# Performance work log

Measured on AMD Instinct MI355X. Metric: run time of the kernel, lower is better.

The kernel has to match this reference:

```python
import jax, jax.numpy as jnp
import numpy as np

INIT_L = 512.0
EPS = 1e-6
N_HEAD = 16


def fire_bias(T, w1, b1, w2, b2, c, L_multiplier):
    # positions and relative distances
    pos = jnp.arange(T, dtype=jnp.float32)
    rel = pos[:, None] - pos[None, :]                      # (T, T)
    threshold = jnp.abs(L_multiplier * INIT_L)
    pos_norm = jnp.maximum(pos, threshold)[:, None]        # (T, 1)
    rel = jnp.log(jnp.abs(c * rel) + 1.0)                  # (T, T)
    pos_norm = jnp.log(jnp.abs(c * pos_norm) + 1.0) + EPS  # (T, 1)
    nd = rel / pos_norm                                    # (T, T)
    # tiny MLP: 1 -> mlp_width -> n_head
    h = jax.nn.relu(nd[..., None] * w1[0] + b1)            # (T, T, 32)
    bias = jnp.einsum('tsw,wh->hts', h, w2) + b2[:, None, None]  # (H, T, T)
    causal = jnp.tril(jnp.ones((T, T), dtype=bool))
    bias = jnp.where(causal[None], bias, -jnp.inf)
    return bias[None]                                      # (1, H, T, T)


def reference(x, Wqkv, bqkv, Wproj, bproj, w1, b1, w2, b2, c_param, L_multiplier):
    B, T, C = x.shape
    H = N_HEAD
    hd = C // H
    qkv = x @ Wqkv + bqkv                                  # (B, T, 3C)
    q, k, v = jnp.split(qkv, 3, axis=-1)
    q = q.reshape(B, T, H, hd).transpose(0, 2, 1, 3)       # (B, H, T, hd)
    k = k.reshape(B, T, H, hd).transpose(0, 2, 1, 3)
    v = v.reshape(B, T, H, hd).transpose(0, 2, 1, 3)
    bias = fire_bias(T, w1, b1, w2, b2, c_param, L_multiplier)  # (1, H, T, T)
    scale = 1.0 / jnp.sqrt(jnp.float32(hd))
    att = jnp.einsum('bhqd,bhkd->bhqk', q, k) * scale + bias
    att = jax.nn.softmax(att, axis=-1)
    y = jnp.einsum('bhqk,bhkd->bhqd', att, v)              # (B, H, T, hd)
    y = y.transpose(0, 2, 1, 3).reshape(B, T, C)
    return y @ Wproj + bproj


def setup_inputs() -> dict:
    key = jax.random.key(0)
    ks = jax.random.split(key, 8)
    B, T, C, H, W = 2, 2048, 1024, 16, 32
    s = 0.02
    return {
        'x': jax.random.normal(ks[0], (B, T, C), jnp.float32),
        'Wqkv': jax.random.normal(ks[1], (C, 3 * C), jnp.float32) * s,
        'bqkv': jnp.zeros((3 * C,), jnp.float32),
        'Wproj': jax.random.normal(ks[2], (C, C), jnp.float32) * s,
        'bproj': jnp.zeros((C,), jnp.float32),
        'w1': jax.random.normal(ks[3], (1, W), jnp.float32),
        'b1': jnp.zeros((W,), jnp.float32),
        'w2': jax.random.normal(ks[4], (W, H), jnp.float32) * 0.1,
        'b2': jnp.zeros((H,), jnp.float32),
        'c_param': jnp.float32(0.1),
        'L_multiplier': jnp.float32(1.0),
    }
```

## Files before the change

kernel.cpp:

```cpp
#include <hip/hip_runtime.h>
#include <cstdint>

typedef unsigned short u16;
typedef unsigned int u32;

typedef short bf16x8 __attribute__((ext_vector_type(8)));
typedef float f32x4 __attribute__((ext_vector_type(4)));

#define LN2 0.69314718055994530942f
#define LOG2E 1.44269504088896340736f
#define INFF __builtin_inff()

__device__ __forceinline__ u16 f2bf(float f) {
  u32 u = __float_as_uint(f);
  u = (u + 0x7fffu + ((u >> 16) & 1u)) >> 16;
  return (u16)u;
}
__device__ __forceinline__ u32 pack2bf(float a, float b) {
  u32 ta = __float_as_uint(a) + 0x8000u;
  u32 tb = __float_as_uint(b) + 0x8000u;
  return __builtin_amdgcn_perm(tb, ta, 0x07060302u);
}

#if __has_builtin(__builtin_amdgcn_global_load_lds)
#define HAVE_GLDS 1
__device__ __forceinline__ void glds16(const u16* g, u16* l) {
  __builtin_amdgcn_global_load_lds((const __attribute__((address_space(1))) void*)g,
                                   (__attribute__((address_space(3))) void*)l, 16, 0, 0);
}
#else
#define HAVE_GLDS 0
#endif

__device__ __forceinline__ u16* swzp(u16* base, int row, int bc) {
  return (u16*)((char*)base + row * 128 + (bc ^ ((row & 7) << 4)));
}


__global__ void k_convert_x(const float* __restrict__ in, u16* __restrict__ out, int n4) {
  int i = blockIdx.x * blockDim.x + threadIdx.x;
  if (i < n4) {
    float4 v = ((const float4*)in)[i];
    ushort4 o;
    o.x = f2bf(v.x); o.y = f2bf(v.y); o.z = f2bf(v.z); o.w = f2bf(v.w);
    ((ushort4*)out)[i] = o;
  }
}

__global__ void k_transpose_bf(const float* __restrict__ in, u16* __restrict__ out, int R, int C) {
  __shared__ float t[32][33];
  int c0 = blockIdx.x * 32, r0 = blockIdx.y * 32;
  int tx = threadIdx.x, ty = threadIdx.y;
#pragma unroll
  for (int k = 0; k < 4; k++) t[ty + 8 * k][tx] = in[(size_t)(r0 + ty + 8 * k) * C + c0 + tx];
  __syncthreads();
#pragma unroll
  for (int k = 0; k < 4; k++) out[(size_t)(c0 + ty + 8 * k) * R + r0 + tx] = f2bf(t[tx][ty + 8 * k]);
}

__global__ void k_tables(const float* __restrict__ cP, const float* __restrict__ lP,
                         float* __restrict__ ig2, float* __restrict__ rl) {
  int t = blockIdx.x * blockDim.x + threadIdx.x;
  float c = fabsf(cP[0]);
  if (t < 2048) {
    float lm = lP[0];
    float thr = fabsf(lm * 512.0f);
    float pn = fmaxf((float)t, thr);
    float den = logf(c * pn + 1.0f) + 1e-6f;
    ig2[t] = LN2 / den;
  }
  if (t < 2112) {
    int d = t - 63;
    if (d < 0) d = 0;
    rl[t] = log2f(c * (float)d + 1.0f);
  }
}

__global__ void k_segments(const float* __restrict__ w1, const float* __restrict__ b1,
                           const float* __restrict__ w2, const float* __restrict__ b2,
                           float* __restrict__ segX, float* __restrict__ segA,
                           float* __restrict__ segB, int* __restrict__ segU) {
  __shared__ float xs[32];
  __shared__ float srt[32];
  __shared__ float uniq[32];
  __shared__ int uCnt;
  int t = threadIdx.x;
  if (t < 32) {
    float w = w1[t], b = b1[t];
    xs[t] = (w != 0.0f) ? (-b / w) : INFF;
  }
  __syncthreads();
  if (t < 32) {
    float x = xs[t];
    int r = 0;
    for (int v = 0; v < 32; v++) {
      float xv = xs[v];
      if (xv < x || (xv == x && v < t)) r++;
    }
    srt[r] = x;
  }
  __syncthreads();
  if (t == 0) {
    int u = 0;
    for (int i = 0; i < 32; i++) {
      float v = srt[i];
      if (v < 3.0e38f && (u == 0 || v != uniq[u - 1])) uniq[u++] = v;
    }
    uCnt = u;
    segU[0] = u;
  }
  __syncthreads();
  int u = uCnt;
  if (t < u) segX[t] = uniq[t];
  for (int idx = t; idx < (u + 1) * 16; idx += blockDim.x) {
    int j = idx >> 4, h = idx & 15;
    float p;
    if (u == 0) p = 0.0f;
    else if (j == 0) p = uniq[0] - 1.0f;
    else if (j == u) p = uniq[u - 1] + 1.0f;
    else p = 0.5f * (uniq[j - 1] + uniq[j]);
    float A = b2[h], B = 0.0f;
    for (int w = 0; w < 32; w++) {
      float w1w = w1[w], b1w = b1[w], w2wh = w2[w * 16 + h];
      if (w1w != 0.0f) {
        if (fmaf(w1w, p, b1w) > 0.0f) { B += w1w * w2wh; A += b1w * w2wh; }
      } else if (b1w > 0.0f) {
        A += b1w * w2wh;
      }
    }
    segA[j * 16 + h] = A;
    segB[j * 16 + h] = B;
  }
}

template <int MODE, int BN>
__launch_bounds__(256, 3)
__global__ void k_gemm(const u16* __restrict__ A, const u16* __restrict__ BT,
                       const float* __restrict__ bias, float* __restrict__ outF,
                       u16* __restrict__ outQ, u16* __restrict__ outK, u16* __restrict__ outV,
                       int M, int N, int K) {
  constexpr int NT = BN / 32;
  constexpr int NCH = BN / 32;
  __shared__ u16 As[128 * 64];
  __shared__ u16 Bs[BN * 64];
  const int tid = threadIdx.x;
  const int lane = tid & 63, wave = tid >> 6;
  const int li = lane & 15, quad = lane >> 4;
  const int wrow = (wave >> 1) * 64, wcol = (wave & 1) * (BN / 2);
  const int rb = blockIdx.y * 128, cb = blockIdx.x * BN;

  f32x4 acc[4][NT];
#pragma unroll
  for (int i = 0; i < 4; i++)
#pragma unroll
    for (int j = 0; j < NT; j++) acc[i][j] = (f32x4){0.f, 0.f, 0.f, 0.f};

#if HAVE_GLDS
  const u16* gA = A + (size_t)(rb + (tid >> 3)) * K + (tid & 7) * 8;
  const u16* gB = BT + (size_t)(cb + (tid >> 3)) * K + (tid & 7) * 8;
  u16* lA = As + wave * 512;
  u16* lB = Bs + wave * 512;

  for (int k0 = 0; k0 < K; k0 += 64) {
    __syncthreads();
#pragma unroll
    for (int ch = 0; ch < 4; ch++) glds16(gA + (size_t)ch * 32 * K + k0, lA + ch * 2048);
#pragma unroll
    for (int ch = 0; ch < NCH; ch++) glds16(gB + (size_t)ch * 32 * K + k0, lB + ch * 2048);
    __syncthreads();
#pragma unroll
    for (int c = 0; c < 2; c++) {
      bf16x8 af[4], bfr[NT];
#pragma unroll
      for (int mt = 0; mt < 4; mt++)
        af[mt] = *(const bf16x8*)(&As[(wrow + mt * 16 + li) * 64 + c * 32 + quad * 8]);
#pragma unroll
      for (int nt = 0; nt < NT; nt++)
        bfr[nt] = *(const bf16x8*)(&Bs[(wcol + nt * 16 + li) * 64 + c * 32 + quad * 8]);
#pragma unroll
      for (int mt = 0; mt < 4; mt++)
#pragma unroll
        for (int nt = 0; nt < NT; nt++)
          acc[mt][nt] = __builtin_amdgcn_mfma_f32_16x16x32_bf16(af[mt], bfr[nt], acc[mt][nt], 0, 0, 0);
    }
  }
#else
  for (int k0 = 0; k0 < K; k0 += 64) {
    __syncthreads();
    for (int idx = tid * 8; idx < 128 * 64; idx += 256 * 8) {
      int rr = idx >> 6, cc = idx & 63;
      *(uint4*)(&As[idx]) = *(const uint4*)(A + (size_t)(rb + rr) * K + k0 + cc);
    }
    for (int idx = tid * 8; idx < BN * 64; idx += 256 * 8) {
      int rr = idx >> 6, cc = idx & 63;
      *(uint4*)(&Bs[idx]) = *(const uint4*)(BT + (size_t)(cb + rr) * K + k0 + cc);
    }
    __syncthreads();
#pragma unroll
    for (int c = 0; c < 2; c++) {
      bf16x8 af[4], bfr[NT];
#pragma unroll
      for (int mt = 0; mt < 4; mt++)
        af[mt] = *(const bf16x8*)(&As[(wrow + mt * 16 + li) * 64 + c * 32 + quad * 8]);
#pragma unroll
      for (int nt = 0; nt < NT; nt++)
        bfr[nt] = *(const bf16x8*)(&Bs[(wcol + nt * 16 + li) * 64 + c * 32 + quad * 8]);
#pragma unroll
      for (int mt = 0; mt < 4; mt++)
#pragma unroll
        for (int nt = 0; nt < NT; nt++)
          acc[mt][nt] = __builtin_amdgcn_mfma_f32_16x16x32_bf16(af[mt], bfr[nt], acc[mt][nt], 0, 0, 0);
    }
  }
#endif

#pragma unroll
  for (int mt = 0; mt < 4; mt++)
#pragma unroll
    for (int nt = 0; nt < NT; nt++)
#pragma unroll
      for (int r = 0; r < 4; r++) {
        int row = rb + wrow + mt * 16 + quad * 4 + r;
        int col = cb + wcol + nt * 16 + li;
        float v = acc[mt][nt][r] + bias[col];
        if (MODE == 0) {
          int b = row >> 11, tt = row & 2047;
          int sel = col >> 10, w = col & 1023, h = w >> 6, dd = w & 63;
          u16* dst = (sel == 0) ? outQ : ((sel == 1) ? outK : outV);
          dst[(size_t)((b * 16 + h) * 2048 + tt) * 64 + dd] = f2bf(v);
        } else {
          outF[(size_t)row * N + col] = v;
        }
      }
}

__launch_bounds__(256, 3)
__global__ void k_attn(const u16* __restrict__ Q, const u16* __restrict__ K,
                       const u16* __restrict__ V, u16* __restrict__ Y,
                       const float* __restrict__ ig2, const float* __restrict__ RL,
                       const float* __restrict__ segX, const float* __restrict__ segA,
                       const float* __restrict__ segB, const int* __restrict__ segU) {
  __shared__ u16 Ks[64 * 64];
  __shared__ u16 Vts[64 * 64];
  __shared__ u16 Ps[64 * 64];
  __shared__ float rls[2112];
  __shared__ float sXl[32];
  __shared__ float sAl[33];
  __shared__ float sBl[33];

  const int xi = blockIdx.x, h = blockIdx.y, b = blockIdx.z;
  const int q0b = xi >> 1;
  const int flip = (xi & 1) ^ ((h >> 3) & 1);
  const int qt = flip ? (31 - q0b) : q0b;

  const int tid = threadIdx.x, lane = tid & 63, wave = tid >> 6;
  const int li = lane & 15, quad = lane >> 4;
  const int bh = b * 16 + h;
  const u16* Qg = Q + (size_t)bh * 2048 * 64;
  const u16* Kg = K + (size_t)bh * 2048 * 64;
  const u16* Vg = V + (size_t)bh * 2048 * 64;

  for (int i = tid; i < 2112; i += 256) rls[i] = RL[i];

  const int u = segU[0];
  float x0 = INFF, A0, B0, A1, B1;
  A0 = segA[h]; B0 = segB[h]; A1 = A0; B1 = B0;
  if (u == 1) { x0 = segX[0]; A1 = segA[16 + h]; B1 = segB[16 + h]; }
  if (u > 1) {
    if (tid < u) sXl[tid] = segX[tid];
    if (tid < u + 1) { sAl[tid] = segA[tid * 16 + h]; sBl[tid] = segB[tid * 16 + h]; }
  }
  const float A0e = A0 * LOG2E, A1e = A1 * LOG2E;
  const float SCL = 0.125f * LOG2E;

  const int qw = qt * 64 + wave * 16;
  const int t = qw + li;
  bf16x8 qf[2];
#pragma unroll
  for (int c = 0; c < 2; c++)
    qf[c] = *(const bf16x8*)(Qg + (size_t)t * 64 + c * 32 + quad * 8);

  const float gI = ig2[t];
  const float x0r = x0 / gI;
  const float B0g = B0 * gI * LOG2E, B1g = B1 * gI * LOG2E;
  float mrow = -INFF, lrow = 0.0f;
  f32x4 oacc[4];
#pragma unroll
  for (int nt = 0; nt < 4; nt++) oacc[nt] = (f32x4){0.f, 0.f, 0.f, 0.f};

  uint4 kv0, kv1, w0, w1;
  {
    const u16* ksrc = Kg + (size_t)(tid >> 2) * 64 + (tid & 3) * 16;
    kv0 = *(const uint4*)(ksrc);
    kv1 = *(const uint4*)(ksrc + 8);
    const u16* vsrc = Vg + (size_t)(2 * (tid & 31)) * 64 + (tid >> 5) * 8;
    w0 = *(const uint4*)(vsrc);
    w1 = *(const uint4*)(vsrc + 64);
  }

  const int krow = tid >> 2, kcol = (tid & 3) * 32;
  const int kkp = tid & 31, d0v = (tid >> 5) * 8;

  for (int kt = 0; kt <= qt; kt++) {
    const int kb = kt * 64;
    __syncthreads();
    *(uint4*)swzp(Ks, krow, kcol) = kv0;
    *(uint4*)swzp(Ks, krow, kcol + 16) = kv1;
    {
      const u16* pw0 = (const u16*)&w0;
      const u16* pw1 = (const u16*)&w1;
#pragma unroll
      for (int j = 0; j < 8; j++)
        *(u32*)swzp(Vts, d0v + j, 4 * kkp) = (u32)pw0[j] | ((u32)pw1[j] << 16);
    }
    __syncthreads();
    if (kt < qt) {
      const u16* ksrc = Kg + (size_t)(kb + 64 + (tid >> 2)) * 64 + (tid & 3) * 16;
      kv0 = *(const uint4*)(ksrc);
      kv1 = *(const uint4*)(ksrc + 8);
      const u16* vsrc = Vg + (size_t)(kb + 64 + 2 * (tid & 31)) * 64 + (tid >> 5) * 8;
      w0 = *(const uint4*)(vsrc);
      w1 = *(const uint4*)(vsrc + 64);
    }

    f32x4 sacc[4];
#pragma unroll
    for (int nt = 0; nt < 4; nt++) sacc[nt] = (f32x4){0.f, 0.f, 0.f, 0.f};
#pragma unroll
    for (int c = 0; c < 2; c++)
#pragma unroll
      for (int nt = 0; nt < 4; nt++) {
        bf16x8 kf = *(const bf16x8*)swzp(Ks, nt * 16 + li, c * 64 + quad * 16);
        sacc[nt] = __builtin_amdgcn_mfma_f32_16x16x32_bf16(kf, qf[c], sacc[nt], 0, 0, 0);
      }

    const int Cbase = t - kb - quad * 4 + 63;
    const float* rp = &rls[Cbase - 51];
    if (u <= 1) {
      const int lim = Cbase - 63;
#pragma unroll
      for (int nt = 0; nt < 4; nt++)
#pragma unroll
        for (int r = 0; r < 4; r++) {
          float rlv = rp[51 - nt * 16 - r];
          bool hi = rlv > x0r;
          float z = fmaf(rlv, hi ? B1g : B0g, hi ? A1e : A0e);
          z = fmaf(sacc[nt][r], SCL, z);
          if (kt == qt) z = (nt * 16 + r > lim) ? -INFF : z;
          sacc[nt][r] = z;
        }
    } else {
      const int lim = Cbase - 63;
#pragma unroll
      for (int nt = 0; nt < 4; nt++)
#pragma unroll
        for (int r = 0; r < 4; r++) {
          float nd = rp[51 - nt * 16 - r] * gI;
          int j = 0;
          for (int i = 0; i < u; i++) j += (nd > sXl[i]) ? 1 : 0;
          float z = (fmaf(nd, sBl[j], sAl[j]) + sacc[nt][r] * 0.125f) * LOG2E;
          if (kt == qt) z = (nt * 16 + r > lim) ? -INFF : z;
          sacc[nt][r] = z;
        }
    }

    f32x4 mm = sacc[0];
#pragma unroll
    for (int nt = 1; nt < 4; nt++)
#pragma unroll
      for (int r = 0; r < 4; r++) mm[r] = fmaxf(mm[r], sacc[nt][r]);
    float vm = fmaxf(fmaxf(mm[0], mm[1]), fmaxf(mm[2], mm[3]));
    vm = fmaxf(vm, __shfl_xor(vm, 16, 64));
    vm = fmaxf(vm, __shfl_xor(vm, 32, 64));
    float mnew = fmaxf(mrow, vm);
    bool grew = mnew > mrow;
    float alpha = __builtin_amdgcn_exp2f(mrow - mnew);
    mrow = mnew;
#pragma unroll
    for (int nt = 0; nt < 4; nt++)
#pragma unroll
      for (int r = 0; r < 4; r++)
        sacc[nt][r] = __builtin_amdgcn_exp2f(sacc[nt][r] - mnew);
    f32x4 sv = (sacc[0] + sacc[1]) + (sacc[2] + sacc[3]);
    float s = (sv[0] + sv[1]) + (sv[2] + sv[3]);
    s += __shfl_xor(s, 16, 64);
    s += __shfl_xor(s, 32, 64);
    lrow = lrow * alpha + s;
    if (__any(grew)) {
#pragma unroll
      for (int nt = 0; nt < 4; nt++)
#pragma unroll
        for (int r = 0; r < 4; r++) oacc[nt][r] *= alpha;
    }

    const int prow = wave * 16 + li;
#pragma unroll
    for (int nt = 0; nt < 4; nt++) {
      uint2 pk;
      pk.x = pack2bf(sacc[nt][0], sacc[nt][1]);
      pk.y = pack2bf(sacc[nt][2], sacc[nt][3]);
      *(uint2*)swzp(Ps, prow, 32 * nt + 8 * quad) = pk;
    }

#pragma unroll
    for (int c = 0; c < 2; c++) {
      bf16x8 pf = *(const bf16x8*)swzp(Ps, prow, c * 64 + quad * 16);
#pragma unroll
      for (int nt = 0; nt < 4; nt++) {
        bf16x8 vf = *(const bf16x8*)swzp(Vts, nt * 16 + li, c * 64 + quad * 16);
        oacc[nt] = __builtin_amdgcn_mfma_f32_16x16x32_bf16(vf, pf, oacc[nt], 0, 0, 0);
      }
    }
  }

  float inv = 1.0f / lrow;
  u16* dst = Y + (size_t)(b * 2048 + t) * 1024 + h * 64 + quad * 4;
#pragma unroll
  for (int nt = 0; nt < 4; nt++) {
    uint2 pk;
    pk.x = pack2bf(oacc[nt][0] * inv, oacc[nt][1] * inv);
    pk.y = pack2bf(oacc[nt][2] * inv, oacc[nt][3] * inv);
    *(uint2*)(dst + nt * 16) = pk;
  }
}

extern "C" void kernel_launch(void* const* d_in, const int* in_sizes, int n_in,
                              void* d_out, int out_size, void* d_ws, size_t ws_size,
                              hipStream_t stream) {
  (void)in_sizes; (void)n_in; (void)out_size; (void)ws_size;
  const float* x = (const float*)d_in[0];
  const float* Wqkv = (const float*)d_in[1];
  const float* bqkv = (const float*)d_in[2];
  const float* Wproj = (const float*)d_in[3];
  const float* bproj = (const float*)d_in[4];
  const float* w1 = (const float*)d_in[5];
  const float* b1 = (const float*)d_in[6];
  const float* w2 = (const float*)d_in[7];
  const float* b2 = (const float*)d_in[8];
  const float* cP = (const float*)d_in[9];
  const float* lP = (const float*)d_in[10];

  char* ws = (char*)d_ws;
  u16* Xbf = (u16*)(ws);
  u16* WqkvT = (u16*)(ws + (size_t)(8 << 20));
  u16* WprojT = (u16*)(ws + (size_t)(14 << 20));
  u16* Qb = (u16*)(ws + (size_t)(16 << 20));
  u16* Kb = (u16*)(ws + (size_t)(24 << 20));
  u16* Vb = (u16*)(ws + (size_t)(32 << 20));
  u16* Yb = (u16*)(ws + (size_t)(40 << 20));
  float* IG = (float*)(ws + (size_t)(48 << 20));
  float* RL = IG + 2048;
  float* SEGX = RL + 2112;
  float* SEGA = SEGX + 32;
  float* SEGB = SEGA + 33 * 16;
  int* SEGU = (int*)(SEGB + 33 * 16);

  k_convert_x<<<4096, 256, 0, stream>>>(x, Xbf, 1048576);
  k_transpose_bf<<<dim3(96, 32), dim3(32, 8), 0, stream>>>(Wqkv, WqkvT, 1024, 3072);
  k_transpose_bf<<<dim3(32, 32), dim3(32, 8), 0, stream>>>(Wproj, WprojT, 1024, 1024);
  k_tables<<<9, 256, 0, stream>>>(cP, lP, IG, RL);
  k_segments<<<1, 64, 0, stream>>>(w1, b1, w2, b2, SEGX, SEGA, SEGB, SEGU);

  k_gemm<0, 128><<<dim3(24, 32), 256, 0, stream>>>(Xbf, WqkvT, bqkv, nullptr, Qb, Kb, Vb,
                                                   4096, 3072, 1024);
  k_attn<<<dim3(32, 16, 2), 256, 0, stream>>>(Qb, Kb, Vb, Yb, IG, RL, SEGX, SEGA, SEGB, SEGU);
  k_gemm<1, 64><<<dim3(16, 32), 256, 0, stream>>>(Yb, WprojT, bproj, (float*)d_out, nullptr,
                                                  nullptr, nullptr, 4096, 1024, 1024);
}
```

Baseline: 243.8 us.

## Split long causal attention query tiles across two blocks with a combine pass

Query tiles 16-31 are now split along the key dimension into two blocks. Each block writes unnormalized fp32 partial outputs plus max and sum statistics, and a new combine kernel merges them into the bf16 output. Short tiles still run as single blocks, so the grid grows from 1024 to 1536 blocks and the work per block is more even, which shortens the tail from the longest causal rows. The cost is an extra kernel launch, fp32 partial traffic through workspace memory, and WprojT moving in the workspace because PO reuses the Xbf region.

```diff
diff --git a/kernel.cpp b/kernel.cpp
--- a/kernel.cpp
+++ b/kernel.cpp
@@ -237,6 +237,7 @@
 __launch_bounds__(256, 3)
 __global__ void k_attn(const u16* __restrict__ Q, const u16* __restrict__ K,
                        const u16* __restrict__ V, u16* __restrict__ Y,
+                       float* __restrict__ PO, float* __restrict__ ML,
                        const float* __restrict__ ig2, const float* __restrict__ RL,
                        const float* __restrict__ segX, const float* __restrict__ segA,
                        const float* __restrict__ segB, const int* __restrict__ segU) {
@@ -249,9 +250,21 @@
   __shared__ float sBl[33];
 
   const int xi = blockIdx.x, h = blockIdx.y, b = blockIdx.z;
-  const int q0b = xi >> 1;
-  const int flip = (xi & 1) ^ ((h >> 3) & 1);
-  const int qt = flip ? (31 - q0b) : q0b;
+  int qt, k0, k1, half, split;
+  if (xi < 32) {
+    qt = 31 - (xi >> 1);
+    half = xi & 1;
+    split = 1;
+    const int h0 = (qt + 2) >> 1;
+    k0 = half ? h0 : 0;
+    k1 = half ? (qt + 1) : h0;
+  } else {
+    qt = 47 - xi;
+    half = 0;
+    split = 0;
+    k0 = 0;
+    k1 = qt + 1;
+  }
 
   const int tid = threadIdx.x, lane = tid & 63, wave = tid >> 6;
   const int li = lane & 15, quad = lane >> 4;
@@ -290,10 +303,10 @@
 
   uint4 kv0, kv1, w0, w1;
   {
-    const u16* ksrc = Kg + (size_t)(tid >> 2) * 64 + (tid & 3) * 16;
+    const u16* ksrc = Kg + (size_t)(k0 * 64 + (tid >> 2)) * 64 + (tid & 3) * 16;
     kv0 = *(const uint4*)(ksrc);
     kv1 = *(const uint4*)(ksrc + 8);
-    const u16* vsrc = Vg + (size_t)(2 * (tid & 31)) * 64 + (tid >> 5) * 8;
+    const u16* vsrc = Vg + (size_t)(k0 * 64 + 2 * (tid & 31)) * 64 + (tid >> 5) * 8;
     w0 = *(const uint4*)(vsrc);
     w1 = *(const uint4*)(vsrc + 64);
   }
@@ -301,7 +314,7 @@
   const int krow = tid >> 2, kcol = (tid & 3) * 32;
   const int kkp = tid & 31, d0v = (tid >> 5) * 8;
 
-  for (int kt = 0; kt <= qt; kt++) {
+  for (int kt = k0; kt < k1; kt++) {
     const int kb = kt * 64;
     __syncthreads();
     *(uint4*)swzp(Ks, krow, kcol) = kv0;
@@ -314,7 +327,7 @@
         *(u32*)swzp(Vts, d0v + j, 4 * kkp) = (u32)pw0[j] | ((u32)pw1[j] << 16);
     }
     __syncthreads();
-    if (kt < qt) {
+    if (kt + 1 < k1) {
       const u16* ksrc = Kg + (size_t)(kb + 64 + (tid >> 2)) * 64 + (tid & 3) * 16;
       kv0 = *(const uint4*)(ksrc);
       kv1 = *(const uint4*)(ksrc + 8);
@@ -413,15 +426,56 @@
     }
   }
 
-  float inv = 1.0f / lrow;
-  u16* dst = Y + (size_t)(b * 2048 + t) * 1024 + h * 64 + quad * 4;
-#pragma unroll
-  for (int nt = 0; nt < 4; nt++) {
-    uint2 pk;
-    pk.x = pack2bf(oacc[nt][0] * inv, oacc[nt][1] * inv);
-    pk.y = pack2bf(oacc[nt][2] * inv, oacc[nt][3] * inv);
-    *(uint2*)(dst + nt * 16) = pk;
-  }
+  if (split) {
+    const int p = bh * 32 + (qt - 16) * 2 + half;
+    const int qr = wave * 16 + li;
+    float* po = PO + (size_t)p * 4096 + (size_t)qr * 64 + quad * 4;
+#pragma unroll
+    for (int nt = 0; nt < 4; nt++) {
+      float4 v4 = make_float4(oacc[nt][0], oacc[nt][1], oacc[nt][2], oacc[nt][3]);
+      *(float4*)(po + nt * 16) = v4;
+    }
+    if (quad == 0) {
+      ML[p * 128 + qr * 2] = mrow;
+      ML[p * 128 + qr * 2 + 1] = lrow;
+    }
+  } else {
+    float inv = 1.0f / lrow;
+    u16* dst = Y + (size_t)(b * 2048 + t) * 1024 + h * 64 + quad * 4;
+#pragma unroll
+    for (int nt = 0; nt < 4; nt++) {
+      uint2 pk;
+      pk.x = pack2bf(oacc[nt][0] * inv, oacc[nt][1] * inv);
+      pk.y = pack2bf(oacc[nt][2] * inv, oacc[nt][3] * inv);
+      *(uint2*)(dst + nt * 16) = pk;
+    }
+  }
+}
+
+__global__ void k_combine(const float* __restrict__ PO, const float* __restrict__ ML,
+                          u16* __restrict__ Y) {
+  const int gid = blockIdx.x * 256 + threadIdx.x;
+  const int d4 = gid & 15;
+  const int row = (gid >> 4) & 1023;
+  const int bh = gid >> 14;
+  const int qt16 = row >> 6, r = row & 63;
+  const int p0 = bh * 32 + qt16 * 2;
+  const float* o0 = PO + (size_t)p0 * 4096 + (size_t)r * 64 + d4 * 4;
+  const float* o1 = o0 + 4096;
+  const float m0 = ML[p0 * 128 + r * 2], l0 = ML[p0 * 128 + r * 2 + 1];
+  const float m1 = ML[(p0 + 1) * 128 + r * 2], l1 = ML[(p0 + 1) * 128 + r * 2 + 1];
+  const float m = fmaxf(m0, m1);
+  const float e0 = __builtin_amdgcn_exp2f(m0 - m);
+  const float e1 = __builtin_amdgcn_exp2f(m1 - m);
+  const float inv = 1.0f / (l0 * e0 + l1 * e1);
+  const float4 a = *(const float4*)o0;
+  const float4 c = *(const float4*)o1;
+  const int t = 1024 + row, b = bh >> 4, h = bh & 15;
+  u16* dst = Y + (size_t)(b * 2048 + t) * 1024 + h * 64 + d4 * 4;
+  uint2 pk;
+  pk.x = pack2bf(fmaf(a.x, e0, c.x * e1) * inv, fmaf(a.y, e0, c.y * e1) * inv);
+  pk.y = pack2bf(fmaf(a.z, e0, c.z * e1) * inv, fmaf(a.w, e0, c.w * e1) * inv);
+  *(uint2*)dst = pk;
 }
 
 extern "C" void kernel_launch(void* const* d_in, const int* in_sizes, int n_in,
@@ -443,7 +497,6 @@
   char* ws = (char*)d_ws;
   u16* Xbf = (u16*)(ws);
   u16* WqkvT = (u16*)(ws + (size_t)(8 << 20));
-  u16* WprojT = (u16*)(ws + (size_t)(14 << 20));
   u16* Qb = (u16*)(ws + (size_t)(16 << 20));
   u16* Kb = (u16*)(ws + (size_t)(24 << 20));
   u16* Vb = (u16*)(ws + (size_t)(32 << 20));
@@ -454,6 +507,9 @@
   float* SEGA = SEGX + 32;
   float* SEGB = SEGA + 33 * 16;
   int* SEGU = (int*)(SEGB + 33 * 16);
+  u16* WprojT = (u16*)(ws + (size_t)(49 << 20));
+  float* PO = (float*)(ws);
+  float* ML = (float*)(ws + (size_t)(51 << 20));
 
   k_convert_x<<<4096, 256, 0, stream>>>(x, Xbf, 1048576);
   k_transpose_bf<<<dim3(96, 32), dim3(32, 8), 0, stream>>>(Wqkv, WqkvT, 1024, 3072);
@@ -463,7 +519,9 @@
 
   k_gemm<0, 128><<<dim3(24, 32), 256, 0, stream>>>(Xbf, WqkvT, bqkv, nullptr, Qb, Kb, Vb,
                                                    4096, 3072, 1024);
-  k_attn<<<dim3(32, 16, 2), 256, 0, stream>>>(Qb, Kb, Vb, Yb, IG, RL, SEGX, SEGA, SEGB, SEGU);
+  k_attn<<<dim3(48, 16, 2), 256, 0, stream>>>(Qb, Kb, Vb, Yb, PO, ML, IG, RL, SEGX, SEGA,
+                                              SEGB, SEGU);
+  k_combine<<<2048, 256, 0, stream>>>(PO, ML, Yb);
   k_gemm<1, 64><<<dim3(16, 32), 256, 0, stream>>>(Yb, WprojT, bproj, (float*)d_out, nullptr,
                                                   nullptr, nullptr, 4096, 1024, 1024);
 }
```

Result: no change. 246.0 us (+0.9%).

## Pre-swizzle K and transpose V in GEMM epilogue; double-buffer attention tiles via direct LDS loads

Applied to the files above, without the earlier changes.

The QKV GEMM epilogue now writes K with an XOR swizzle and V already transposed and swizzled, so the attention kernel can copy tiles straight from global memory into LDS with global_load_lds instead of staging them through registers and scattering. K and V LDS buffers are doubled so the next tile loads while the current one is computed, and one of the two __syncthreads per iteration goes away. A specialized bias path skips the piecewise select when both segments are effectively the same. The change raises LDS use per block, which may reduce occupancy, and relies on the epilogue layout matching the swizzle the attention kernel reads with.

```diff
diff --git a/kernel.cpp b/kernel.cpp
--- a/kernel.cpp
+++ b/kernel.cpp
@@ -20,6 +20,9 @@
   u32 ta = __float_as_uint(a) + 0x8000u;
   u32 tb = __float_as_uint(b) + 0x8000u;
   return __builtin_amdgcn_perm(tb, ta, 0x07060302u);
+}
+__device__ __forceinline__ u32 pack2bf_rne(float a, float b) {
+  return (u32)f2bf(a) | ((u32)f2bf(b) << 16);
 }
 
 #if __has_builtin(__builtin_amdgcn_global_load_lds)
@@ -31,6 +34,15 @@
 #else
 #define HAVE_GLDS 0
 #endif
+
+__device__ __forceinline__ void stage1k(const u16* gperlane, u16* lwave, int lane) {
+#if HAVE_GLDS
+  (void)lane;
+  glds16(gperlane, lwave);
+#else
+  *(uint4*)(lwave + lane * 8) = *(const uint4*)gperlane;
+#endif
+}
 
 __device__ __forceinline__ u16* swzp(u16* base, int row, int bc) {
   return (u16*)((char*)base + row * 128 + (bc ^ ((row & 7) << 4)));
@@ -217,31 +229,48 @@
 #pragma unroll
   for (int mt = 0; mt < 4; mt++)
 #pragma unroll
-    for (int nt = 0; nt < NT; nt++)
-#pragma unroll
-      for (int r = 0; r < 4; r++) {
-        int row = rb + wrow + mt * 16 + quad * 4 + r;
-        int col = cb + wcol + nt * 16 + li;
-        float v = acc[mt][nt][r] + bias[col];
-        if (MODE == 0) {
-          int b = row >> 11, tt = row & 2047;
-          int sel = col >> 10, w = col & 1023, h = w >> 6, dd = w & 63;
-          u16* dst = (sel == 0) ? outQ : ((sel == 1) ? outK : outV);
-          dst[(size_t)((b * 16 + h) * 2048 + tt) * 64 + dd] = f2bf(v);
+    for (int nt = 0; nt < NT; nt++) {
+      const int col = cb + wcol + nt * 16 + li;
+      const int row0 = rb + wrow + mt * 16 + quad * 4;
+      float v[4];
+#pragma unroll
+      for (int r = 0; r < 4; r++) v[r] = acc[mt][nt][r] + bias[col];
+      if (MODE == 0) {
+        const int bb = row0 >> 11, tt0 = row0 & 2047;
+        const int sel = col >> 10, w = col & 1023, hh = w >> 6, dd = w & 63;
+        if (sel == 0) {
+          u16* dst = outQ + ((size_t)((bb * 16 + hh) * 2048 + tt0)) * 64 + dd;
+#pragma unroll
+          for (int r = 0; r < 4; r++) dst[(size_t)r * 64] = f2bf(v[r]);
+        } else if (sel == 1) {
+          u16* base = outK + ((size_t)((bb * 16 + hh) * 2048 + tt0)) * 64;
+#pragma unroll
+          for (int r = 0; r < 4; r++) {
+            int tt = tt0 + r;
+            base[(size_t)r * 64 + (dd ^ (((tt & 7)) << 3))] = f2bf(v[r]);
+          }
         } else {
-          outF[(size_t)row * N + col] = v;
+          u16* vrow = outV + ((size_t)((bb * 16 + hh) * 64 + dd)) * 2048;
+          uint2 pk;
+          pk.x = pack2bf_rne(v[0], v[1]);
+          pk.y = pack2bf_rne(v[2], v[3]);
+          *(uint2*)(vrow + (tt0 ^ ((dd & 7) << 3))) = pk;
         }
+      } else {
+#pragma unroll
+        for (int r = 0; r < 4; r++) outF[(size_t)(row0 + r) * N + col] = v[r];
       }
+    }
 }
 
 __launch_bounds__(256, 3)
 __global__ void k_attn(const u16* __restrict__ Q, const u16* __restrict__ K,
-                       const u16* __restrict__ V, u16* __restrict__ Y,
+                       const u16* __restrict__ Vt, u16* __restrict__ Y,
                        const float* __restrict__ ig2, const float* __restrict__ RL,
                        const float* __restrict__ segX, const float* __restrict__ segA,
                        const float* __restrict__ segB, const int* __restrict__ segU) {
-  __shared__ u16 Ks[64 * 64];
-  __shared__ u16 Vts[64 * 64];
+  __shared__ u16 KsB[2 * 64 * 64];
+  __shared__ u16 VtsB[2 * 64 * 64];
   __shared__ u16 Ps[64 * 64];
   __shared__ float rls[2112];
   __shared__ float sXl[32];
@@ -258,7 +287,7 @@
   const int bh = b * 16 + h;
   const u16* Qg = Q + (size_t)bh * 2048 * 64;
   const u16* Kg = K + (size_t)bh * 2048 * 64;
-  const u16* Vg = V + (size_t)bh * 2048 * 64;
+  const u16* Vg = Vt + (size_t)bh * 64 * 2048;
 
   for (int i = tid; i < 2112; i += 256) rls[i] = RL[i];
 
@@ -273,8 +302,7 @@
   const float A0e = A0 * LOG2E, A1e = A1 * LOG2E;
   const float SCL = 0.125f * LOG2E;
 
-  const int qw = qt * 64 + wave * 16;
-  const int t = qw + li;
+  const int t = qt * 64 + wave * 16 + li;
   bf16x8 qf[2];
 #pragma unroll
   for (int c = 0; c < 2; c++)
@@ -283,45 +311,36 @@
   const float gI = ig2[t];
   const float x0r = x0 / gI;
   const float B0g = B0 * gI * LOG2E, B1g = B1 * gI * LOG2E;
+  const bool uniB = (u <= 1) && (x0r <= 0.0f) && (A0e == A1e);
   float mrow = -INFF, lrow = 0.0f;
   f32x4 oacc[4];
 #pragma unroll
   for (int nt = 0; nt < 4; nt++) oacc[nt] = (f32x4){0.f, 0.f, 0.f, 0.f};
 
-  uint4 kv0, kv1, w0, w1;
-  {
-    const u16* ksrc = Kg + (size_t)(tid >> 2) * 64 + (tid & 3) * 16;
-    kv0 = *(const uint4*)(ksrc);
-    kv1 = *(const uint4*)(ksrc + 8);
-    const u16* vsrc = Vg + (size_t)(2 * (tid & 31)) * 64 + (tid >> 5) * 8;
-    w0 = *(const uint4*)(vsrc);
-    w1 = *(const uint4*)(vsrc + 64);
-  }
-
-  const int krow = tid >> 2, kcol = (tid & 3) * 32;
-  const int kkp = tid & 31, d0v = (tid >> 5) * 8;
+  const u16* kgB = Kg + (size_t)(wave * 16 + (lane >> 3)) * 64 + (lane & 7) * 8;
+  const u16* vgB = Vg + (size_t)(wave * 16 + (lane >> 3)) * 2048 + (lane & 7) * 8;
+
+  auto stage = [&](int buf, int kt2) {
+    u16* kd = KsB + buf * 4096 + wave * 1024;
+    const u16* kg = kgB + (size_t)kt2 * 4096;
+    stage1k(kg, kd, lane);
+    stage1k(kg + 8 * 64, kd + 512, lane);
+    u16* vd = VtsB + buf * 4096 + wave * 1024;
+    const u16* vg = vgB + kt2 * 64;
+    stage1k(vg, vd, lane);
+    stage1k(vg + 8 * 2048, vd + 512, lane);
+  };
+
+  stage(0, 0);
+  int cur = 0;
 
   for (int kt = 0; kt <= qt; kt++) {
     const int kb = kt * 64;
     __syncthreads();
-    *(uint4*)swzp(Ks, krow, kcol) = kv0;
-    *(uint4*)swzp(Ks, krow, kcol + 16) = kv1;
-    {
-      const u16* pw0 = (const u16*)&w0;
-      const u16* pw1 = (const u16*)&w1;
-#pragma unroll
-      for (int j = 0; j < 8; j++)
-        *(u32*)swzp(Vts, d0v + j, 4 * kkp) = (u32)pw0[j] | ((u32)pw1[j] << 16);
-    }
-    __syncthreads();
-    if (kt < qt) {
-      const u16* ksrc = Kg + (size_t)(kb + 64 + (tid >> 2)) * 64 + (tid & 3) * 16;
-      kv0 = *(const uint4*)(ksrc);
-      kv1 = *(const uint4*)(ksrc + 8);
-      const u16* vsrc = Vg + (size_t)(kb + 64 + 2 * (tid & 31)) * 64 + (tid >> 5) * 8;
-      w0 = *(const uint4*)(vsrc);
-      w1 = *(const uint4*)(vsrc + 64);
-    }
+    if (kt < qt) stage(cur ^ 1, kt + 1);
+
+    u16* KsT = KsB + cur * 4096;
+    u16* VtT = VtsB + cur * 4096;
 
     f32x4 sacc[4];
 #pragma unroll
@@ -330,14 +349,23 @@
     for (int c = 0; c < 2; c++)
 #pragma unroll
       for (int nt = 0; nt < 4; nt++) {
-        bf16x8 kf = *(const bf16x8*)swzp(Ks, nt * 16 + li, c * 64 + quad * 16);
+        bf16x8 kf = *(const bf16x8*)swzp(KsT, nt * 16 + li, c * 64 + quad * 16);
         sacc[nt] = __builtin_amdgcn_mfma_f32_16x16x32_bf16(kf, qf[c], sacc[nt], 0, 0, 0);
       }
 
     const int Cbase = t - kb - quad * 4 + 63;
     const float* rp = &rls[Cbase - 51];
-    if (u <= 1) {
-      const int lim = Cbase - 63;
+    const int lim = Cbase - 63;
+    if (uniB) {
+#pragma unroll
+      for (int nt = 0; nt < 4; nt++)
+#pragma unroll
+        for (int r = 0; r < 4; r++) {
+          float z = fmaf(rp[51 - nt * 16 - r], B1g, sacc[nt][r] * SCL);
+          if (kt == qt) z = (nt * 16 + r > lim) ? -INFF : z;
+          sacc[nt][r] = z;
+        }
+    } else if (u <= 1) {
 #pragma unroll
       for (int nt = 0; nt < 4; nt++)
 #pragma unroll
@@ -350,7 +378,6 @@
           sacc[nt][r] = z;
         }
     } else {
-      const int lim = Cbase - 63;
 #pragma unroll
       for (int nt = 0; nt < 4; nt++)
 #pragma unroll
@@ -407,10 +434,11 @@
       bf16x8 pf = *(const bf16x8*)swzp(Ps, prow, c * 64 + quad * 16);
 #pragma unroll
       for (int nt = 0; nt < 4; nt++) {
-        bf16x8 vf = *(const bf16x8*)swzp(Vts, nt * 16 + li, c * 64 + quad * 16);
+        bf16x8 vf = *(const bf16x8*)swzp(VtT, nt * 16 + li, c * 64 + quad * 16);
         oacc[nt] = __builtin_amdgcn_mfma_f32_16x16x32_bf16(vf, pf, oacc[nt], 0, 0, 0);
       }
     }
+    cur ^= 1;
   }
 
   float inv = 1.0f / lrow;
```

Result: no change. 239.9 us (-1.6%).
